# Performance work log

Hardware: AMD Instinct MI355X
Metric: run time of the kernel (lower is better)

Reference implementation:

```python
import jax, jax.numpy as jnp
import numpy as np

S, B, D, H = 2048, 2, 1024, 16
DK = D // H
SCALE = 1.0 / np.sqrt(DK)


def setup_inputs() -> dict:
    key = jax.random.key(0)
    ks = jax.random.split(key, 12)
    std = 1.0 / np.sqrt(D)
    inp = {
        "query": jax.random.normal(ks[0], (S, B, D), jnp.float32),
        "key": jax.random.normal(ks[1], (S, B, D), jnp.float32),
        "value": jax.random.normal(ks[2], (S, B, D), jnp.float32),
        # causal mask [S, S, 1]; mask[i, j] = 1 iff query i may attend key j
        "mask": jnp.tril(jnp.ones((S, S), jnp.bool_))[:, :, None],
        "Wq": jax.random.normal(ks[3], (D, D), jnp.float32) * std,
        "bq": jax.random.normal(ks[4], (D,), jnp.float32) * std,
        "Wk": jax.random.normal(ks[5], (D, D), jnp.float32) * std,
        "bk": jax.random.normal(ks[6], (D,), jnp.float32) * std,
        "Wv": jax.random.normal(ks[7], (D, D), jnp.float32) * std,
        "bv": jax.random.normal(ks[8], (D,), jnp.float32) * std,
        "Wo": jax.random.normal(ks[9], (D, D), jnp.float32) * std,
        "bo": jax.random.normal(ks[10], (D,), jnp.float32) * std,
    }
    return inp


def _proj(x, W, b):
    # nn.Linear: x @ W.T + b, then split into heads -> [S, B, H, DK]
    s, bsz, _ = x.shape
    y = jnp.einsum('sbd,ed->sbe', x, W) + b
    return y.reshape(s, bsz, H, DK)


def reference(query, key, value, mask, Wq, bq, Wk, bk, Wv, bv, Wo, bo):
    q = _proj(query, Wq, bq)   # [S,B,H,DK]
    k = _proj(key, Wk, bk)
    v = _proj(value, Wv, bv)
    scores = jnp.einsum('ibhd,jbhd->ijbh', q, k) * SCALE  # [S,S,B,H]
    m = mask[:, :, :, None]  # [S,S,1,1] or [S,S,B,1]
    scores = jnp.where(m, scores, jnp.float32(-1e9))
    attn = jax.nn.softmax(scores, axis=1)
    x = jnp.einsum('ijbh,jbhd->ibhd', attn, v)  # [S,B,H,DK]
    x = x.reshape(S, B, D)
    return jnp.einsum('sbd,ed->sbe', x, Wo) + bo
```

## Files before the change

### kernel.cpp

```cpp
#include <hip/hip_runtime.h>
#include <stdint.h>

#define S_LEN 2048
#define BATCH 2
#define DMODEL 1024
#define NHEAD 16
#define DHEAD 64
#define QSCALE 0.18033688011112042f

typedef float f32x4 __attribute__((ext_vector_type(4)));
typedef float f32x16 __attribute__((ext_vector_type(16)));
typedef __bf16 bf16x8 __attribute__((ext_vector_type(8)));
typedef unsigned short u16x8 __attribute__((ext_vector_type(8)));

#define EXP2(x) exp2f(x)

__device__ __forceinline__ unsigned short f2bf(float f) {
  union { float f; unsigned int u; } v;
  v.f = f;
  unsigned int u = v.u;
  return (unsigned short)((u + 0x7fffu + ((u >> 16) & 1u)) >> 16);
}

__device__ __forceinline__ unsigned pk2(float lo, float hi_) {
  union { __bf16 h[2]; unsigned u; } c;
  c.h[0] = (__bf16)lo; c.h[1] = (__bf16)hi_;
  return c.u;
}

__device__ __forceinline__ void gld16(const void* g, void* l) {
  __builtin_amdgcn_global_load_lds((__attribute__((address_space(1))) void*)(g),
                                   (__attribute__((address_space(3))) void*)(l),
                                   16, 0, 0);
}

__global__ void cvt_w_kernel(const float* __restrict__ wq, const float* __restrict__ wk,
                             const float* __restrict__ wv, const float* __restrict__ wosrc,
                             unsigned short* __restrict__ wp, unsigned short* __restrict__ wo) {
  const int b = blockIdx.x;
  const int z = b >> 10, local = b & 1023;
  const float* src = (z == 0 ? wq : (z == 1 ? wk : (z == 2 ? wv : wosrc))) + (size_t)local * 1024;
  unsigned short* dst = (z < 3 ? wp + (size_t)z * 1048576 : wo) + (size_t)local * 1024;
  const int i = threadIdx.x * 4;
  const float4 val = *(const float4*)(src + i);
  ushort4 o;
  o.x = f2bf(val.x); o.y = f2bf(val.y); o.z = f2bf(val.z); o.w = f2bf(val.w);
  *(ushort4*)(dst + i) = o;
}

template <int MODE>
__global__ __launch_bounds__(256, 2) void gemm_bt(
    const float* __restrict__ Aq, const float* __restrict__ Akk, const float* __restrict__ Avv,
    const unsigned short* __restrict__ Ab,
    const unsigned short* __restrict__ Wbase,
    const float* __restrict__ bias0, const float* __restrict__ bias1,
    const float* __restrict__ bias2,
    unsigned short* __restrict__ qw, unsigned short* __restrict__ kw,
    unsigned short* __restrict__ vtw, float* __restrict__ outp) {
  constexpr int N = DMODEL;
  constexpr int K = DMODEL;
  constexpr int AST = (MODE == 0) ? 40 : 32;
  __shared__ unsigned short At[128 * AST];
  __shared__ unsigned short Bt[128 * 32];

  const int m0 = blockIdx.x * 128;
  const int n0 = blockIdx.y * 128;
  const int z = (MODE == 0) ? blockIdx.z : 0;
  const unsigned short* W = Wbase + (size_t)z * N * K;
  const float* bias = (z == 0 ? bias0 : (z == 1 ? bias1 : bias2));

  const int tid = threadIdx.x;
  const int w = tid >> 6, l = tid & 63;
  const int wr = w >> 1, wc = w & 1;
  const int lr = l & 15, lg = l >> 4;

  const int srow = tid >> 2;
  const int scol = (tid & 3) * 8;

  const int arow = tid >> 1;
  const int aks = (tid & 1) << 4;
  const float* Af = (MODE == 0) ? (z == 0 ? Aq : (z == 1 ? Akk : Avv)) : nullptr;
  const float* abase = (MODE == 0) ? (Af + (size_t)(m0 + arow) * K + aks) : nullptr;

  float4 av[4];
  if (MODE == 0) {
#pragma unroll
    for (int c = 0; c < 4; ++c) av[c] = *(const float4*)(abase + 4 * c);
  }

  f32x4 acc[4][4] = {};

  for (int k0 = 0; k0 < K; k0 += 32) {
    if (k0) __syncthreads();
    if (MODE == 0) {
      union { __bf16 h[8]; u16x8 v; } c0, c1;
#pragma unroll
      for (int j = 0; j < 4; ++j) { c0.h[j] = (__bf16)av[0][j]; c0.h[4 + j] = (__bf16)av[1][j]; }
#pragma unroll
      for (int j = 0; j < 4; ++j) { c1.h[j] = (__bf16)av[2][j]; c1.h[4 + j] = (__bf16)av[3][j]; }
      *(u16x8*)&At[arow * AST + aks] = c0.v;
      *(u16x8*)&At[arow * AST + aks + 8] = c1.v;
    } else {
      gld16(Ab + (size_t)(m0 + srow) * K + k0 + scol, (char*)At + w * 1024);
      gld16(Ab + (size_t)(m0 + 64 + srow) * K + k0 + scol, (char*)At + w * 1024 + 4096);
    }
    gld16(W + (size_t)(n0 + srow) * K + k0 + scol, (char*)Bt + w * 1024);
    gld16(W + (size_t)(n0 + 64 + srow) * K + k0 + scol, (char*)Bt + w * 1024 + 4096);
    __syncthreads();

    if (MODE == 0 && k0 + 32 < K) {
#pragma unroll
      for (int c = 0; c < 4; ++c) av[c] = *(const float4*)(abase + k0 + 32 + 4 * c);
    }

    bf16x8 af[4], bfr[4];
#pragma unroll
    for (int mt = 0; mt < 4; ++mt)
      af[mt] = *(const bf16x8*)&At[(wr * 64 + mt * 16 + lr) * AST + lg * 8];
#pragma unroll
    for (int nt = 0; nt < 4; ++nt)
      bfr[nt] = *(const bf16x8*)&Bt[(wc * 64 + nt * 16 + lr) * 32 + lg * 8];
#pragma unroll
    for (int mt = 0; mt < 4; ++mt)
#pragma unroll
      for (int nt = 0; nt < 4; ++nt)
        acc[mt][nt] = __builtin_amdgcn_mfma_f32_16x16x32_bf16(af[mt], bfr[nt], acc[mt][nt], 0, 0, 0);
  }

#pragma unroll
  for (int mt = 0; mt < 4; ++mt) {
#pragma unroll
    for (int nt = 0; nt < 4; ++nt) {
#pragma unroll
      for (int r = 0; r < 4; ++r) {
        const int gm = m0 + wr * 64 + mt * 16 + lg * 4 + r;
        const int gn = n0 + wc * 64 + nt * 16 + lr;
        float v = acc[mt][nt][r] + bias[gn];
        if (MODE == 1) {
          outp[(size_t)gm * N + gn] = v;
        } else {
          if (z == 0) v *= QSCALE;
          const int s = gm >> 1, bb = gm & 1;
          const int h = gn >> 6, dk = gn & 63;
          const int bh = bb * NHEAD + h;
          const unsigned short bv_ = f2bf(v);
          if (z == 0)
            qw[((size_t)bh * S_LEN + s) * DHEAD + dk] = bv_;
          else if (z == 1)
            kw[((size_t)bh * S_LEN + s) * DHEAD + dk] = bv_;
          else
            vtw[((size_t)bh * DHEAD + dk) * S_LEN + s] = bv_;
        }
      }
    }
  }
}

__global__ __launch_bounds__(512) void attn_kernel(
    const unsigned short* __restrict__ qw, const unsigned short* __restrict__ kw,
    const unsigned short* __restrict__ vtw, unsigned short* __restrict__ x2) {
  __shared__ unsigned short lds_all[32768];
  __shared__ float mlscr[3][2][64][2];

  const int bh = blockIdx.x;
  const int xq = blockIdx.y;
  const int bb = bh >> 4, h = bh & 15;
  const int tid = threadIdx.x;
  const int w = tid >> 6, l = tid & 63;
  const int q5 = l & 31, hi = l >> 5;
  const int quar = w >> 1, wh = w & 1;

  const size_t qkbase = (size_t)bh * S_LEN * DHEAD;
  const size_t vbase = (size_t)bh * DHEAD * S_LEN;

  const int qtA = 31 - xq, qtB = xq;
  const int nA = qtA + 1, nB = qtB + 1;
  const int sA = (nA + 3) >> 2;
  const int sTot = sA + ((nB + 3) >> 2);

  auto stage = [&](int t0, int lim) {
#pragma unroll
    for (int r = 0; r < 4; ++r) {
      const int g = w * 4 + r;
      const int ti = g >> 3;
      const int row = ((g & 7) << 3) + (l >> 3);
      const int ch = (l & 7) ^ (row & 7);
      int t = t0 + ti;
      if (t >= lim) t = lim - 1;
      gld16(kw + qkbase + (size_t)(t * 64 + row) * DHEAD + ch * 8,
            (char*)lds_all + g * 1024);
      gld16(vtw + vbase + (size_t)row * S_LEN + t * 64 + ch * 8,
            (char*)lds_all + 32768 + g * 1024);
    }
  };

  int qt = qtA;
  int qrow = qt * 64 + wh * 32 + q5;
  bf16x8 qf[4];
#pragma unroll
  for (int d = 0; d < 4; ++d)
    qf[d] = *(const bf16x8*)&qw[qkbase + (size_t)qrow * DHEAD + d * 16 + hi * 8];

  f32x16 oacc0, oacc1;
#pragma unroll
  for (int r = 0; r < 16; ++r) { oacc0[r] = 0.f; oacc1[r] = 0.f; }
  float mrun = -1e30f, lrun = 0.f;

  stage(0, nA);
  __syncthreads();

  const char* kb = (const char*)lds_all + quar * 8192;
  const char* vb = (const char*)lds_all + 32768 + quar * 8192;

  for (int s = 0; s < sTot; ++s) {
    const bool phA = (s < sA);
    const int myt = (phA ? 4 * s : 4 * (s - sA)) + quar;
    const int lim = phA ? nA : nB;

    if (myt < lim) {
      const int kt = myt;

      f32x16 scA, scB;
#pragma unroll
      for (int r = 0; r < 16; ++r) { scA[r] = 0.f; scB[r] = 0.f; }
      __builtin_amdgcn_s_setprio(1);
#pragma unroll
      for (int d = 0; d < 4; ++d) {
        const int ch = (2 * d + hi) ^ (q5 & 7);
        const bf16x8 kfA = *(const bf16x8*)(kb + q5 * 128 + ch * 16);
        const bf16x8 kfB = *(const bf16x8*)(kb + (32 + q5) * 128 + ch * 16);
        scA = __builtin_amdgcn_mfma_f32_32x32x16_bf16(kfA, qf[d], scA, 0, 0, 0);
        scB = __builtin_amdgcn_mfma_f32_32x32x16_bf16(kfB, qf[d], scB, 0, 0, 0);
      }
      __builtin_amdgcn_s_setprio(0);

      if (kt == qt) {
        const int qloc = wh * 32 + q5;
#pragma unroll
        for (int r = 0; r < 16; ++r) {
          const int kv = (r & 3) + 8 * (r >> 2) + 4 * hi;
          if (kv > qloc) scA[r] = -1e9f;
          if (kv + 32 > qloc) scB[r] = -1e9f;
        }
      }

      float mx[8];
#pragma unroll
      for (int j = 0; j < 8; ++j)
        mx[j] = fmaxf(fmaxf(scA[j], scA[j + 8]), fmaxf(scB[j], scB[j + 8]));
#pragma unroll
      for (int j = 0; j < 4; ++j) mx[j] = fmaxf(mx[j], mx[j + 4]);
      float tmax = fmaxf(fmaxf(mx[0], mx[1]), fmaxf(mx[2], mx[3]));
      tmax = fmaxf(tmax, __shfl_xor(tmax, 32, 64));
      if (!__all(tmax <= mrun + 8.0f)) {
        const float mnew = fmaxf(mrun, tmax);
        const float resc = EXP2(mrun - mnew);
        mrun = mnew;
        lrun *= resc;
#pragma unroll
        for (int r = 0; r < 16; ++r) { oacc0[r] *= resc; oacc1[r] *= resc; }
      }
#pragma unroll
      for (int r = 0; r < 16; ++r) scA[r] = EXP2(scA[r] - mrun);
#pragma unroll
      for (int r = 0; r < 16; ++r) scB[r] = EXP2(scB[r] - mrun);
      float sm[8];
#pragma unroll
      for (int j = 0; j < 8; ++j)
        sm[j] = (scA[j] + scA[j + 8]) + (scB[j] + scB[j + 8]);
#pragma unroll
      for (int j = 0; j < 4; ++j) sm[j] += sm[j + 4];
      float rsum = (sm[0] + sm[1]) + (sm[2] + sm[3]);
      rsum += __shfl_xor(rsum, 32, 64);
      lrun += rsum;

      unsigned pk[2][8];
#pragma unroll
      for (int g = 0; g < 4; ++g) {
        pk[0][2 * g]     = pk2(scA[4 * g],     scA[4 * g + 1]);
        pk[0][2 * g + 1] = pk2(scA[4 * g + 2], scA[4 * g + 3]);
        pk[1][2 * g]     = pk2(scB[4 * g],     scB[4 * g + 1]);
        pk[1][2 * g + 1] = pk2(scB[4 * g + 2], scB[4 * g + 3]);
      }

#pragma unroll
      for (int t = 0; t < 4; ++t) {
        const int c = t >> 1, ks = t & 1;
        const unsigned o0 = pk[c][4 * ks + 0], o1 = pk[c][4 * ks + 1];
        const unsigned o2 = pk[c][4 * ks + 2], o3 = pk[c][4 * ks + 3];
        const unsigned ea = (unsigned)__shfl_xor((int)(hi ? o0 : o2), 32, 64);
        const unsigned eb = (unsigned)__shfl_xor((int)(hi ? o1 : o3), 32, 64);
        union { unsigned u[4]; bf16x8 v; } pb;
        pb.u[0] = hi ? ea : o0;
        pb.u[1] = hi ? eb : o1;
        pb.u[2] = hi ? o2 : ea;
        pb.u[3] = hi ? o3 : eb;
        const int vch = (2 * t + hi) ^ (q5 & 7);
        const bf16x8 vf0 = *(const bf16x8*)(vb + q5 * 128 + vch * 16);
        const bf16x8 vf1 = *(const bf16x8*)(vb + (32 + q5) * 128 + vch * 16);
        __builtin_amdgcn_s_setprio(1);
        oacc0 = __builtin_amdgcn_mfma_f32_32x32x16_bf16(vf0, pb.v, oacc0, 0, 0, 0);
        oacc1 = __builtin_amdgcn_mfma_f32_32x32x16_bf16(vf1, pb.v, oacc1, 0, 0, 0);
        __builtin_amdgcn_s_setprio(0);
      }
    }

    if (s == sA - 1 || s == sTot - 1) {
      __syncthreads();
      float* scr = (float*)lds_all;
      const int kx = l & 7;
      if (quar != 0) {
        f32x4* d4 = (f32x4*)(scr + (size_t)(((quar - 1) * 2 + wh) * 64 + l) * 32);
#pragma unroll
        for (int c = 0; c < 4; ++c) {
          f32x4 ch_;
#pragma unroll
          for (int j = 0; j < 4; ++j) ch_[j] = oacc0[c * 4 + j];
          d4[c ^ kx] = ch_;
        }
#pragma unroll
        for (int c = 0; c < 4; ++c) {
          f32x4 ch_;
#pragma unroll
          for (int j = 0; j < 4; ++j) ch_[j] = oacc1[c * 4 + j];
          d4[(4 + c) ^ kx] = ch_;
        }
        mlscr[quar - 1][wh][l][0] = mrun;
        mlscr[quar - 1][wh][l][1] = lrun;
      }
      __syncthreads();
      if (quar == 0) {
        float ms = mrun, lm = lrun;
        f32x16 a0 = oacc0, a1 = oacc1;
#pragma unroll
        for (int p = 1; p <= 3; ++p) {
          const f32x4* s4 = (const f32x4*)(scr + (size_t)(((p - 1) * 2 + wh) * 64 + l) * 32);
          const float mp = mlscr[p - 1][wh][l][0], lp = mlscr[p - 1][wh][l][1];
          const float mn = fmaxf(ms, mp);
          const float c0 = EXP2(ms - mn), c1 = EXP2(mp - mn);
#pragma unroll
          for (int g = 0; g < 4; ++g) {
            const f32x4 p0 = s4[g ^ kx];
            const f32x4 p1 = s4[(4 + g) ^ kx];
#pragma unroll
            for (int j = 0; j < 4; ++j) {
              a0[4 * g + j] = a0[4 * g + j] * c0 + p0[j] * c1;
              a1[4 * g + j] = a1[4 * g + j] * c0 + p1[j] * c1;
            }
          }
          lm = lm * c0 + lp * c1;
          ms = mn;
        }
        const float invl = 1.0f / lm;
        const size_t obase = ((size_t)qrow * BATCH + bb) * DMODEL + h * DHEAD;
#pragma unroll
        for (int g = 0; g < 4; ++g) {
          const int d0 = 8 * g + 4 * hi;
          ushort4 s0, s1;
          s0.x = f2bf(a0[4 * g + 0] * invl);
          s0.y = f2bf(a0[4 * g + 1] * invl);
          s0.z = f2bf(a0[4 * g + 2] * invl);
          s0.w = f2bf(a0[4 * g + 3] * invl);
          s1.x = f2bf(a1[4 * g + 0] * invl);
          s1.y = f2bf(a1[4 * g + 1] * invl);
          s1.z = f2bf(a1[4 * g + 2] * invl);
          s1.w = f2bf(a1[4 * g + 3] * invl);
          *(ushort4*)(x2 + obase + d0) = s0;
          *(ushort4*)(x2 + obase + 32 + d0) = s1;
        }
      }
      if (s == sA - 1) {
        qt = qtB;
        qrow = qt * 64 + wh * 32 + q5;
#pragma unroll
        for (int d = 0; d < 4; ++d)
          qf[d] = *(const bf16x8*)&qw[qkbase + (size_t)qrow * DHEAD + d * 16 + hi * 8];
#pragma unroll
        for (int r = 0; r < 16; ++r) { oacc0[r] = 0.f; oacc1[r] = 0.f; }
        mrun = -1e30f;
        lrun = 0.f;
      }
    }

    __syncthreads();
    if (s + 1 < sTot) {
      int t0, lim2;
      if (s + 1 < sA) { t0 = 4 * (s + 1); lim2 = nA; }
      else { t0 = 4 * (s + 1 - sA); lim2 = nB; }
      stage(t0, lim2);
    }
    __syncthreads();
  }
}

extern "C" void kernel_launch(void* const* d_in, const int* in_sizes, int n_in,
                              void* d_out, int out_size, void* d_ws, size_t ws_size,
                              hipStream_t stream) {
  (void)in_sizes; (void)n_in; (void)out_size;
  if (ws_size < (size_t)67108864) return;

  const float* query = (const float*)d_in[0];
  const float* key_  = (const float*)d_in[1];
  const float* value = (const float*)d_in[2];
  const float* Wq = (const float*)d_in[4];
  const float* bq = (const float*)d_in[5];
  const float* Wk = (const float*)d_in[6];
  const float* bk = (const float*)d_in[7];
  const float* Wv = (const float*)d_in[8];
  const float* bv = (const float*)d_in[9];
  const float* Wo = (const float*)d_in[10];
  const float* bo = (const float*)d_in[11];

  char* ws = (char*)d_ws;
  unsigned short* wp  = (unsigned short*)(ws);
  unsigned short* wo  = (unsigned short*)(ws + 6291456);
  unsigned short* qws = (unsigned short*)(ws + 8388608);
  unsigned short* kws = (unsigned short*)(ws + 16777216);
  unsigned short* vtw = (unsigned short*)(ws + 25165824);
  unsigned short* x2  = (unsigned short*)(ws + 33554432);

  cvt_w_kernel<<<4096, 256, 0, stream>>>(Wq, Wk, Wv, Wo, wp, wo);

  gemm_bt<0><<<dim3(32, 8, 3), 256, 0, stream>>>(query, key_, value, nullptr, wp,
                                                 bq, bk, bv, qws, kws, vtw, nullptr);
  attn_kernel<<<dim3(32, 16), 512, 0, stream>>>(qws, kws, vtw, x2);
  gemm_bt<1><<<dim3(32, 8, 1), 256, 0, stream>>>(nullptr, nullptr, nullptr, x2, wo,
                                                 bo, bo, bo, nullptr, nullptr, nullptr,
                                                 (float*)d_out);
}
```

Baseline: 141.0 us.

## Double-buffer K tiles in LDS and load V fragments directly from global

The attention kernel now keeps two LDS buffers for K tiles and issues the next tile's async global-to-LDS loads at the start of each iteration, so the copy overlaps the current compute. V no longer goes through LDS: each lane reads its V^T fragments straight from global memory into registers, split into two batches around the softmax so the load latency is hidden. A launch bound of 4 is added to pressure register allocation. In exchange, V reads lose LDS sharing across the waves of a block, and the extra register arrays may cause spills or lower occupancy.

```diff
diff --git a/kernel.cpp b/kernel.cpp
--- a/kernel.cpp
+++ b/kernel.cpp
@@ -32,6 +32,11 @@
   __builtin_amdgcn_global_load_lds((__attribute__((address_space(1))) void*)(g),
                                    (__attribute__((address_space(3))) void*)(l),
                                    16, 0, 0);
+}
+
+__device__ __forceinline__ float xswapf(float x) { return __shfl_xor(x, 32, 64); }
+__device__ __forceinline__ unsigned xswapu(unsigned x) {
+  return (unsigned)__shfl_xor((int)x, 32, 64);
 }
 
 __global__ void cvt_w_kernel(const float* __restrict__ wq, const float* __restrict__ wk,
@@ -156,10 +161,10 @@
   }
 }
 
-__global__ __launch_bounds__(512) void attn_kernel(
+__global__ __launch_bounds__(512, 4) void attn_kernel(
     const unsigned short* __restrict__ qw, const unsigned short* __restrict__ kw,
     const unsigned short* __restrict__ vtw, unsigned short* __restrict__ x2) {
-  __shared__ unsigned short lds_all[32768];
+  __shared__ unsigned short klds[2][4][4096];
   __shared__ float mlscr[3][2][64][2];
 
   const int bh = blockIdx.x;
@@ -175,22 +180,20 @@
 
   const int qtA = 31 - xq, qtB = xq;
   const int nA = qtA + 1, nB = qtB + 1;
-  const int sA = (nA + 3) >> 2;
-  const int sTot = sA + ((nB + 3) >> 2);
-
-  auto stage = [&](int t0, int lim) {
+  const int sA_ = (nA + 3) >> 2;
+  const int sTot = sA_ + ((nB + 3) >> 2);
+
+  auto stage = [&](int t0, int lim2, int buf) {
 #pragma unroll
     for (int r = 0; r < 4; ++r) {
-      const int g = w * 4 + r;
-      const int ti = g >> 3;
-      const int row = ((g & 7) << 3) + (l >> 3);
-      const int ch = (l & 7) ^ (row & 7);
+      const int slot = w * 4 + r;
+      const int ti = slot >> 3;
+      const int row = ((slot & 7) << 3) + (l >> 3);
+      const int ch = (l & 7) ^ (l >> 3);
       int t = t0 + ti;
-      if (t >= lim) t = lim - 1;
+      if (t >= lim2) t = lim2 - 1;
       gld16(kw + qkbase + (size_t)(t * 64 + row) * DHEAD + ch * 8,
-            (char*)lds_all + g * 1024);
-      gld16(vtw + vbase + (size_t)row * S_LEN + t * 64 + ch * 8,
-            (char*)lds_all + 32768 + g * 1024);
+            (char*)klds + buf * 32768 + ti * 8192 + (slot & 7) * 1024);
     }
   };
 
@@ -206,19 +209,34 @@
   for (int r = 0; r < 16; ++r) { oacc0[r] = 0.f; oacc1[r] = 0.f; }
   float mrun = -1e30f, lrun = 0.f;
 
-  stage(0, nA);
+  stage(0, nA, 0);
   __syncthreads();
 
-  const char* kb = (const char*)lds_all + quar * 8192;
-  const char* vb = (const char*)lds_all + 32768 + quar * 8192;
-
   for (int s = 0; s < sTot; ++s) {
-    const bool phA = (s < sA);
-    const int myt = (phA ? 4 * s : 4 * (s - sA)) + quar;
+    const int cur = s & 1;
+    const bool mergeIter = (s == sA_ - 1) || (s == sTot - 1);
+    if (!mergeIter) {
+      int t0, lim2;
+      if (s + 1 < sA_) { t0 = 4 * (s + 1); lim2 = nA; }
+      else { t0 = 4 * (s + 1 - sA_); lim2 = nB; }
+      stage(t0, lim2, cur ^ 1);
+    }
+
+    const bool phA = (s < sA_);
+    const int myt = (phA ? 4 * s : 4 * (s - sA_)) + quar;
     const int lim = phA ? nA : nB;
 
     if (myt < lim) {
       const int kt = myt;
+      const char* kb = (const char*)klds + cur * 32768 + quar * 8192;
+
+      const unsigned short* vrow0 = vtw + vbase + (size_t)q5 * S_LEN + kt * 64 + 8 * hi;
+      const unsigned short* vrow1 = vtw + vbase + (size_t)(32 + q5) * S_LEN + kt * 64 + 8 * hi;
+      bf16x8 vf0[4], vf1[4];
+      vf0[0] = *(const bf16x8*)(vrow0);
+      vf1[0] = *(const bf16x8*)(vrow1);
+      vf0[1] = *(const bf16x8*)(vrow0 + 16);
+      vf1[1] = *(const bf16x8*)(vrow1 + 16);
 
       f32x16 scA, scB;
 #pragma unroll
@@ -251,7 +269,7 @@
 #pragma unroll
       for (int j = 0; j < 4; ++j) mx[j] = fmaxf(mx[j], mx[j + 4]);
       float tmax = fmaxf(fmaxf(mx[0], mx[1]), fmaxf(mx[2], mx[3]));
-      tmax = fmaxf(tmax, __shfl_xor(tmax, 32, 64));
+      tmax = fmaxf(tmax, xswapf(tmax));
       if (!__all(tmax <= mrun + 8.0f)) {
         const float mnew = fmaxf(mrun, tmax);
         const float resc = EXP2(mrun - mnew);
@@ -271,8 +289,13 @@
 #pragma unroll
       for (int j = 0; j < 4; ++j) sm[j] += sm[j + 4];
       float rsum = (sm[0] + sm[1]) + (sm[2] + sm[3]);
-      rsum += __shfl_xor(rsum, 32, 64);
+      rsum += xswapf(rsum);
       lrun += rsum;
+
+      vf0[2] = *(const bf16x8*)(vrow0 + 32);
+      vf1[2] = *(const bf16x8*)(vrow1 + 32);
+      vf0[3] = *(const bf16x8*)(vrow0 + 48);
+      vf1[3] = *(const bf16x8*)(vrow1 + 48);
 
       unsigned pk[2][8];
 #pragma unroll
@@ -288,26 +311,23 @@
         const int c = t >> 1, ks = t & 1;
         const unsigned o0 = pk[c][4 * ks + 0], o1 = pk[c][4 * ks + 1];
         const unsigned o2 = pk[c][4 * ks + 2], o3 = pk[c][4 * ks + 3];
-        const unsigned ea = (unsigned)__shfl_xor((int)(hi ? o0 : o2), 32, 64);
-        const unsigned eb = (unsigned)__shfl_xor((int)(hi ? o1 : o3), 32, 64);
+        const unsigned ea = xswapu(hi ? o0 : o2);
+        const unsigned eb = xswapu(hi ? o1 : o3);
         union { unsigned u[4]; bf16x8 v; } pb;
         pb.u[0] = hi ? ea : o0;
         pb.u[1] = hi ? eb : o1;
         pb.u[2] = hi ? o2 : ea;
         pb.u[3] = hi ? o3 : eb;
-        const int vch = (2 * t + hi) ^ (q5 & 7);
-        const bf16x8 vf0 = *(const bf16x8*)(vb + q5 * 128 + vch * 16);
-        const bf16x8 vf1 = *(const bf16x8*)(vb + (32 + q5) * 128 + vch * 16);
         __builtin_amdgcn_s_setprio(1);
-        oacc0 = __builtin_amdgcn_mfma_f32_32x32x16_bf16(vf0, pb.v, oacc0, 0, 0, 0);
-        oacc1 = __builtin_amdgcn_mfma_f32_32x32x16_bf16(vf1, pb.v, oacc1, 0, 0, 0);
+        oacc0 = __builtin_amdgcn_mfma_f32_32x32x16_bf16(vf0[t], pb.v, oacc0, 0, 0, 0);
+        oacc1 = __builtin_amdgcn_mfma_f32_32x32x16_bf16(vf1[t], pb.v, oacc1, 0, 0, 0);
         __builtin_amdgcn_s_setprio(0);
       }
     }
 
-    if (s == sA - 1 || s == sTot - 1) {
+    if (mergeIter) {
       __syncthreads();
-      float* scr = (float*)lds_all;
+      float* scr = (float*)klds;
       const int kx = l & 7;
       if (quar != 0) {
         f32x4* d4 = (f32x4*)(scr + (size_t)(((quar - 1) * 2 + wh) * 64 + l) * 32);
@@ -369,7 +389,7 @@
           *(ushort4*)(x2 + obase + 32 + d0) = s1;
         }
       }
-      if (s == sA - 1) {
+      if (s == sA_ - 1) {
         qt = qtB;
         qrow = qt * 64 + wh * 32 + q5;
 #pragma unroll
@@ -380,14 +400,8 @@
         mrun = -1e30f;
         lrun = 0.f;
       }
-    }
-
-    __syncthreads();
-    if (s + 1 < sTot) {
-      int t0, lim2;
-      if (s + 1 < sA) { t0 = 4 * (s + 1); lim2 = nA; }
-      else { t0 = 4 * (s + 1 - sA); lim2 = nB; }
-      stage(t0, lim2);
+      __syncthreads();
+      if (s + 1 < sTot) stage(0, nB, cur ^ 1);
     }
     __syncthreads();
   }
```

Measured after the change: 199.3 us. 41.4% more time.
